# Kernel tuning notes

Measured on AMD Instinct MI355X. Metric: run time of the kernel, lower is better.

The kernel has to match this reference:

```python
import jax, jax.numpy as jnp
import numpy as np

D_IN, H, H1, H2 = 50, 64, 32, 1

def setup_inputs() -> dict:
    key = jax.random.key(0)
    ks = jax.random.split(key, 13)
    s = 1.0 / np.sqrt(H)
    u = lambda k, shp: jax.random.uniform(k, shp, jnp.float32, -s, s)
    x = jax.random.normal(ks[0], (512, 2048, D_IN), jnp.float32)
    return {
        "x": x,
        "W_ih0": u(ks[1], (H, D_IN)), "W_hh0": u(ks[2], (H, H)),
        "b_ih0": u(ks[3], (H,)),      "b_hh0": u(ks[4], (H,)),
        "W_ih1": u(ks[5], (H, H)),    "W_hh1": u(ks[6], (H, H)),
        "b_ih1": u(ks[7], (H,)),      "b_hh1": u(ks[8], (H,)),
        "W1": u(ks[9], (H1, H)),      "b1": u(ks[10], (H1,)),
        "W2": u(ks[11], (H2, H1)),    "b2": u(ks[12], (H2,)),
    }

def reference(x, W_ih0, W_hh0, b_ih0, b_hh0, W_ih1, W_hh1, b_ih1, b_hh1, W1, b1, W2, b2):
    B = x.shape[0]
    # Precompute input projections for layer 0 for all timesteps: [S, B, H]
    xt = jnp.swapaxes(x, 0, 1)  # [S, B, D_IN]
    x_proj0 = jnp.einsum('sbd,hd->sbh', xt, W_ih0) + b_ih0 + b_hh0

    h0 = jnp.zeros((B, H), x.dtype)

    def step(carry, xp):
        h1, h2 = carry
        h1 = jnp.tanh(xp + h1 @ W_hh0.T)
        h2 = jnp.tanh(h1 @ W_ih1.T + b_ih1 + h2 @ W_hh1.T + b_hh1)
        return (h1, h2), None

    (h1f, h2f), _ = jax.lax.scan(step, (h0, h0), x_proj0)
    hidden = jax.nn.relu(h2f @ W1.T + b1)
    return jax.nn.sigmoid(hidden @ W2.T + b2)
```

## Files before the change

kernel.cpp:

```cpp
#include <hip/hip_runtime.h>

#define S_LEN 2048
#define DIN   50
#define H     64

__device__ __forceinline__ float tanh_fast(float v) {
    float e = __builtin_amdgcn_exp2f(v * 2.885390082f);
    return 1.0f - 2.0f * __builtin_amdgcn_rcpf(e + 1.0f);
}

__device__ __forceinline__ float red4(float v) {
#if __has_builtin(__builtin_amdgcn_permlane16_swap) && __has_builtin(__builtin_amdgcn_permlane32_swap)
    typedef unsigned u2 __attribute__((ext_vector_type(2)));
    u2 r = __builtin_amdgcn_permlane16_swap(__float_as_uint(v), __float_as_uint(v), false, false);
    float s = __uint_as_float(r[0]) + __uint_as_float(r[1]);
    u2 q = __builtin_amdgcn_permlane32_swap(__float_as_uint(s), __float_as_uint(s), false, false);
    return __uint_as_float(q[0]) + __uint_as_float(q[1]);
#else
    v += __shfl_xor(v, 16, 64);
    v += __shfl_xor(v, 32, 64);
    return v;
#endif
}

__global__ __launch_bounds__(512)
__attribute__((amdgpu_waves_per_eu(4, 4)))
void rnn_fused(const float* __restrict__ x,
               const float* __restrict__ W_ih0, const float* __restrict__ W_hh0,
               const float* __restrict__ b_ih0, const float* __restrict__ b_hh0,
               const float* __restrict__ W_ih1, const float* __restrict__ W_hh1,
               const float* __restrict__ b_ih1, const float* __restrict__ b_hh1,
               const float* __restrict__ W1, const float* __restrict__ b1,
               const float* __restrict__ W2, const float* __restrict__ b2,
               float* __restrict__ out)
{
    const int b    = blockIdx.x;
    const int tid  = threadIdx.x;
    const int lane = tid & 63;
    const int w    = __builtin_amdgcn_readfirstlane(tid >> 6);
    const bool isA = (w < 4);
    const int wr   = isA ? w : w - 4;
    const int j    = lane & 15;
    const int kg   = lane >> 4;
    const int outj = 16 * wr + j;

    __shared__ __align__(16) float xs[2][4][16];
    __shared__ __align__(16) float h1s[2][H];
    __shared__ __align__(16) float h2s[2][H];

    float arrP[16], arrQ[16];
    if (isA) {
        #pragma unroll
        for (int i = 0; i < 16; ++i) {
            int c = 13 * kg + i;
            arrP[i] = (i < 13 && c < DIN) ? W_ih0[outj * DIN + c] : 0.0f;
            arrQ[i] = W_hh0[outj * H + 16 * kg + i];
        }
    } else {
        #pragma unroll
        for (int i = 0; i < 16; ++i) {
            arrP[i] = W_ih1[outj * H + 16 * kg + i];
            arrQ[i] = W_hh1[outj * H + 16 * kg + i];
        }
    }
    const float bias = isA ? (b_ih0[outj] + b_hh0[outj])
                           : (b_ih1[outj] + b_hh1[outj]);

    const float* __restrict__ xrow = x + (size_t)b * (size_t)(S_LEN * DIN);

    const int  scol = 13 * kg + j;
    const bool sval = (tid < 64) && (j < 13) && (scol < DIN);

    if (tid < 64) xs[0][kg][j] = sval ? xrow[scol] : 0.0f;
    float pfA = sval ? xrow[DIN + scol] : 0.0f;
    float pfB = sval ? xrow[2 * DIN + scol] : 0.0f;
    const float* xpf = xrow + 3 * DIN + scol;

    if (tid < 64) { h1s[1][lane] = 0.0f; h2s[1][lane] = 0.0f; }
    __syncthreads();

    auto iter = [&](int t, int cur, int prv) {
        if (isA) {
            if (t < S_LEN) {
                float s1[16], s2[16];
                #pragma unroll
                for (int q = 0; q < 4; ++q)
                    *(float4*)&s1[4 * q] = *(const float4*)&xs[cur][kg][4 * q];
                #pragma unroll
                for (int q = 0; q < 4; ++q)
                    *(float4*)&s2[4 * q] = *(const float4*)&h1s[prv][16 * kg + 4 * q];
                float a0 = 0, a1 = 0, a2 = 0, a3 = 0;
                #pragma unroll
                for (int q = 0; q < 4; ++q) {
                    a0 = fmaf(s1[4 * q + 0], arrP[4 * q + 0], a0);
                    a1 = fmaf(s1[4 * q + 1], arrP[4 * q + 1], a1);
                    a2 = fmaf(s1[4 * q + 2], arrP[4 * q + 2], a2);
                    a3 = fmaf(s1[4 * q + 3], arrP[4 * q + 3], a3);
                }
                #pragma unroll
                for (int q = 0; q < 4; ++q) {
                    a0 = fmaf(s2[4 * q + 0], arrQ[4 * q + 0], a0);
                    a1 = fmaf(s2[4 * q + 1], arrQ[4 * q + 1], a1);
                    a2 = fmaf(s2[4 * q + 2], arrQ[4 * q + 2], a2);
                    a3 = fmaf(s2[4 * q + 3], arrQ[4 * q + 3], a3);
                }
                float h1n = tanh_fast(red4((a0 + a1) + (a2 + a3)) + bias);
                if (kg == 0) h1s[cur][outj] = h1n;
                if (tid < 64) xs[prv][kg][j] = pfA;
                pfA = pfB;
                pfB = (sval && (t + 3) < S_LEN) ? *xpf : 0.0f;
                xpf += DIN;
            }
        } else {
            if (t >= 1) {
                float s1[16], s2[16];
                #pragma unroll
                for (int q = 0; q < 4; ++q)
                    *(float4*)&s1[4 * q] = *(const float4*)&h1s[prv][16 * kg + 4 * q];
                #pragma unroll
                for (int q = 0; q < 4; ++q)
                    *(float4*)&s2[4 * q] = *(const float4*)&h2s[cur][16 * kg + 4 * q];
                float c0 = 0, c1 = 0, c2 = 0, c3 = 0;
                #pragma unroll
                for (int q = 0; q < 4; ++q) {
                    c0 = fmaf(s1[4 * q + 0], arrP[4 * q + 0], c0);
                    c1 = fmaf(s1[4 * q + 1], arrP[4 * q + 1], c1);
                    c2 = fmaf(s1[4 * q + 2], arrP[4 * q + 2], c2);
                    c3 = fmaf(s1[4 * q + 3], arrP[4 * q + 3], c3);
                }
                #pragma unroll
                for (int q = 0; q < 4; ++q) {
                    c0 = fmaf(s2[4 * q + 0], arrQ[4 * q + 0], c0);
                    c1 = fmaf(s2[4 * q + 1], arrQ[4 * q + 1], c1);
                    c2 = fmaf(s2[4 * q + 2], arrQ[4 * q + 2], c2);
                    c3 = fmaf(s2[4 * q + 3], arrQ[4 * q + 3], c3);
                }
                float h2n = tanh_fast(red4((c0 + c1) + (c2 + c3)) + bias);
                if (kg == 0) h2s[prv][outj] = h2n;
            }
        }
    };

    for (int t = 0; t < S_LEN; t += 2) {
        iter(t, 0, 1);
        __syncthreads();
        iter(t + 1, 1, 0);
        __syncthreads();
    }
    iter(S_LEN, 0, 1);
    __syncthreads();

    if (tid < 64) {
        float hv = 0.0f;
        if (lane < 32) {
            float acc = b1[lane];
            #pragma unroll
            for (int k = 0; k < H; ++k)
                acc = fmaf(h2s[1][k], W1[lane * H + k], acc);
            hv = fmaxf(acc, 0.0f) * W2[lane];
        }
        #pragma unroll
        for (int off = 32; off; off >>= 1)
            hv += __shfl_xor(hv, off, 64);
        if (lane == 0)
            out[b] = 1.0f / (1.0f + __expf(-(hv + b2[0])));
    }
}

extern "C" void kernel_launch(void* const* d_in, const int* in_sizes, int n_in,
                              void* d_out, int out_size, void* d_ws, size_t ws_size,
                              hipStream_t stream) {
    const float* x     = (const float*)d_in[0];
    const float* W_ih0 = (const float*)d_in[1];
    const float* W_hh0 = (const float*)d_in[2];
    const float* b_ih0 = (const float*)d_in[3];
    const float* b_hh0 = (const float*)d_in[4];
    const float* W_ih1 = (const float*)d_in[5];
    const float* W_hh1 = (const float*)d_in[6];
    const float* b_ih1 = (const float*)d_in[7];
    const float* b_hh1 = (const float*)d_in[8];
    const float* W1    = (const float*)d_in[9];
    const float* b1    = (const float*)d_in[10];
    const float* W2    = (const float*)d_in[11];
    const float* b2    = (const float*)d_in[12];
    float* out = (float*)d_out;

    rnn_fused<<<dim3(512), dim3(512), 0, stream>>>(
        x, W_ih0, W_hh0, b_ih0, b_hh0,
        W_ih1, W_hh1, b_ih1, b_hh1,
        W1, b1, W2, b2, out);
}
```

Before: 1.087 ms.

## Rewrite RNN recurrence as single-wave bf16 MFMA kernel batching 16 sequences

Replaces the 512-thread-per-sequence FP32 dot-product kernel with a one-wavefront block that handles 16 batch rows and runs both RNN layers through bf16 16x16x32 MFMA instructions. Weights are held as bf16 register fragments, and hidden states go through a small LDS transpose each step to re-form A fragments. The next x projection is computed one step ahead and inputs are prefetched from global memory. This removes block-wide barriers and cuts the grid from 512 to 32 blocks. The cost is bf16 rounding of weights and hidden states across 2048 steps, plus very low parallelism (32 waves) on a large GPU.

Measured after the change: 1.900 ms. 74.8% more time.

```diff
diff --git a/kernel.cpp b/kernel.cpp
--- a/kernel.cpp
+++ b/kernel.cpp
@@ -3,6 +3,33 @@
 #define S_LEN 2048
 #define DIN   50
 #define H     64
+#define ROWS  16
+#define XSTR  (S_LEN * DIN)
+
+typedef short bf16x8 __attribute__((ext_vector_type(8)));
+typedef float f32x4  __attribute__((ext_vector_type(4)));
+
+union U8 { bf16x8 v; unsigned u[4]; };
+
+__device__ __forceinline__ unsigned cvt2bf(float lo, float hi) {
+    unsigned r;
+    asm("v_cvt_pk_bf16_f32 %0, %1, %2" : "=v"(r) : "v"(lo), "v"(hi));
+    return r;
+}
+
+__device__ __forceinline__ bf16x8 pack8v(float4 a, float4 b) {
+    U8 u;
+    u.u[0] = cvt2bf(a.x, a.y); u.u[1] = cvt2bf(a.z, a.w);
+    u.u[2] = cvt2bf(b.x, b.y); u.u[3] = cvt2bf(b.z, b.w);
+    return u.v;
+}
+
+__device__ __forceinline__ bf16x8 pack8a(const float f[8]) {
+    U8 u;
+    u.u[0] = cvt2bf(f[0], f[1]); u.u[1] = cvt2bf(f[2], f[3]);
+    u.u[2] = cvt2bf(f[4], f[5]); u.u[3] = cvt2bf(f[6], f[7]);
+    return u.v;
+}
 
 __device__ __forceinline__ float tanh_fast(float v) {
     float e = __builtin_amdgcn_exp2f(v * 2.885390082f);
@@ -23,147 +50,204 @@
 #endif
 }
 
-__global__ __launch_bounds__(512)
-__attribute__((amdgpu_waves_per_eu(4, 4)))
-void rnn_fused(const float* __restrict__ x,
-               const float* __restrict__ W_ih0, const float* __restrict__ W_hh0,
-               const float* __restrict__ b_ih0, const float* __restrict__ b_hh0,
-               const float* __restrict__ W_ih1, const float* __restrict__ W_hh1,
-               const float* __restrict__ b_ih1, const float* __restrict__ b_hh1,
-               const float* __restrict__ W1, const float* __restrict__ b1,
-               const float* __restrict__ W2, const float* __restrict__ b2,
-               float* __restrict__ out)
+__device__ __forceinline__ bf16x8 load_bfrag(const float* __restrict__ W, int ld, int kmax,
+                                             int n, int ks) {
+    float f[8];
+    #pragma unroll
+    for (int j = 0; j < 8; ++j)
+        f[j] = (ks + j < kmax) ? W[n * ld + ks + j] : 0.0f;
+    return pack8a(f);
+}
+
+#define MFMA(a, b, c) __builtin_amdgcn_mfma_f32_16x16x32_bf16(a, b, c, 0, 0, 0)
+
+__global__ __launch_bounds__(64)
+__attribute__((amdgpu_waves_per_eu(1, 1)))
+void rnn_mfma(const float* __restrict__ x,
+              const float* __restrict__ W_ih0, const float* __restrict__ W_hh0,
+              const float* __restrict__ b_ih0, const float* __restrict__ b_hh0,
+              const float* __restrict__ W_ih1, const float* __restrict__ W_hh1,
+              const float* __restrict__ b_ih1, const float* __restrict__ b_hh1,
+              const float* __restrict__ W1, const float* __restrict__ b1,
+              const float* __restrict__ W2, const float* __restrict__ b2,
+              float* __restrict__ out)
 {
-    const int b    = blockIdx.x;
-    const int tid  = threadIdx.x;
-    const int lane = tid & 63;
-    const int w    = __builtin_amdgcn_readfirstlane(tid >> 6);
-    const bool isA = (w < 4);
-    const int wr   = isA ? w : w - 4;
-    const int j    = lane & 15;
-    const int kg   = lane >> 4;
-    const int outj = 16 * wr + j;
-
-    __shared__ __align__(16) float xs[2][4][16];
-    __shared__ __align__(16) float h1s[2][H];
-    __shared__ __align__(16) float h2s[2][H];
-
-    float arrP[16], arrQ[16];
-    if (isA) {
-        #pragma unroll
-        for (int i = 0; i < 16; ++i) {
-            int c = 13 * kg + i;
-            arrP[i] = (i < 13 && c < DIN) ? W_ih0[outj * DIN + c] : 0.0f;
-            arrQ[i] = W_hh0[outj * H + 16 * kg + i];
-        }
-    } else {
-        #pragma unroll
-        for (int i = 0; i < 16; ++i) {
-            arrP[i] = W_ih1[outj * H + 16 * kg + i];
-            arrQ[i] = W_hh1[outj * H + 16 * kg + i];
-        }
-    }
-    const float bias = isA ? (b_ih0[outj] + b_hh0[outj])
-                           : (b_ih1[outj] + b_hh1[outj]);
-
-    const float* __restrict__ xrow = x + (size_t)b * (size_t)(S_LEN * DIN);
-
-    const int  scol = 13 * kg + j;
-    const bool sval = (tid < 64) && (j < 13) && (scol < DIN);
-
-    if (tid < 64) xs[0][kg][j] = sval ? xrow[scol] : 0.0f;
-    float pfA = sval ? xrow[DIN + scol] : 0.0f;
-    float pfB = sval ? xrow[2 * DIN + scol] : 0.0f;
-    const float* xpf = xrow + 3 * DIN + scol;
-
-    if (tid < 64) { h1s[1][lane] = 0.0f; h2s[1][lane] = 0.0f; }
-    __syncthreads();
-
-    auto iter = [&](int t, int cur, int prv) {
-        if (isA) {
-            if (t < S_LEN) {
-                float s1[16], s2[16];
-                #pragma unroll
-                for (int q = 0; q < 4; ++q)
-                    *(float4*)&s1[4 * q] = *(const float4*)&xs[cur][kg][4 * q];
-                #pragma unroll
-                for (int q = 0; q < 4; ++q)
-                    *(float4*)&s2[4 * q] = *(const float4*)&h1s[prv][16 * kg + 4 * q];
-                float a0 = 0, a1 = 0, a2 = 0, a3 = 0;
-                #pragma unroll
-                for (int q = 0; q < 4; ++q) {
-                    a0 = fmaf(s1[4 * q + 0], arrP[4 * q + 0], a0);
-                    a1 = fmaf(s1[4 * q + 1], arrP[4 * q + 1], a1);
-                    a2 = fmaf(s1[4 * q + 2], arrP[4 * q + 2], a2);
-                    a3 = fmaf(s1[4 * q + 3], arrP[4 * q + 3], a3);
-                }
-                #pragma unroll
-                for (int q = 0; q < 4; ++q) {
-                    a0 = fmaf(s2[4 * q + 0], arrQ[4 * q + 0], a0);
-                    a1 = fmaf(s2[4 * q + 1], arrQ[4 * q + 1], a1);
-                    a2 = fmaf(s2[4 * q + 2], arrQ[4 * q + 2], a2);
-                    a3 = fmaf(s2[4 * q + 3], arrQ[4 * q + 3], a3);
-                }
-                float h1n = tanh_fast(red4((a0 + a1) + (a2 + a3)) + bias);
-                if (kg == 0) h1s[cur][outj] = h1n;
-                if (tid < 64) xs[prv][kg][j] = pfA;
-                pfA = pfB;
-                pfB = (sval && (t + 3) < S_LEN) ? *xpf : 0.0f;
-                xpf += DIN;
-            }
-        } else {
-            if (t >= 1) {
-                float s1[16], s2[16];
-                #pragma unroll
-                for (int q = 0; q < 4; ++q)
-                    *(float4*)&s1[4 * q] = *(const float4*)&h1s[prv][16 * kg + 4 * q];
-                #pragma unroll
-                for (int q = 0; q < 4; ++q)
-                    *(float4*)&s2[4 * q] = *(const float4*)&h2s[cur][16 * kg + 4 * q];
-                float c0 = 0, c1 = 0, c2 = 0, c3 = 0;
-                #pragma unroll
-                for (int q = 0; q < 4; ++q) {
-                    c0 = fmaf(s1[4 * q + 0], arrP[4 * q + 0], c0);
-                    c1 = fmaf(s1[4 * q + 1], arrP[4 * q + 1], c1);
-                    c2 = fmaf(s1[4 * q + 2], arrP[4 * q + 2], c2);
-                    c3 = fmaf(s1[4 * q + 3], arrP[4 * q + 3], c3);
-                }
-                #pragma unroll
-                for (int q = 0; q < 4; ++q) {
-                    c0 = fmaf(s2[4 * q + 0], arrQ[4 * q + 0], c0);
-                    c1 = fmaf(s2[4 * q + 1], arrQ[4 * q + 1], c1);
-                    c2 = fmaf(s2[4 * q + 2], arrQ[4 * q + 2], c2);
-                    c3 = fmaf(s2[4 * q + 3], arrQ[4 * q + 3], c3);
-                }
-                float h2n = tanh_fast(red4((c0 + c1) + (c2 + c3)) + bias);
-                if (kg == 0) h2s[prv][outj] = h2n;
-            }
-        }
-    };
-
-    for (int t = 0; t < S_LEN; t += 2) {
-        iter(t, 0, 1);
-        __syncthreads();
-        iter(t + 1, 1, 0);
-        __syncthreads();
-    }
-    iter(S_LEN, 0, 1);
-    __syncthreads();
-
-    if (tid < 64) {
-        float hv = 0.0f;
-        if (lane < 32) {
-            float acc = b1[lane];
-            #pragma unroll
-            for (int k = 0; k < H; ++k)
-                acc = fmaf(h2s[1][k], W1[lane * H + k], acc);
-            hv = fmaxf(acc, 0.0f) * W2[lane];
-        }
-        #pragma unroll
-        for (int off = 32; off; off >>= 1)
-            hv += __shfl_xor(hv, off, 64);
-        if (lane == 0)
-            out[b] = 1.0f / (1.0f + __expf(-(hv + b2[0])));
+    const int blk  = blockIdx.x;
+    const int lane = threadIdx.x & 63;
+    const int li   = lane & 15;
+    const int lg   = lane >> 4;
+
+    __shared__ __align__(16) float hb1[ROWS][68];
+    __shared__ __align__(16) float hb2[ROWS][68];
+
+    bf16x8 whh0B[4][2], wih1B[4][2], whh1B[4][2], wih0B[4][2];
+    f32x4  b0c[4], b1c[4];
+    #pragma unroll
+    for (int nt = 0; nt < 4; ++nt) {
+        const int n = 16 * nt + li;
+        #pragma unroll
+        for (int kf = 0; kf < 2; ++kf) {
+            const int ks = 32 * kf + lg * 8;
+            whh0B[nt][kf] = load_bfrag(W_hh0, H,   H,   n, ks);
+            wih1B[nt][kf] = load_bfrag(W_ih1, H,   H,   n, ks);
+            whh1B[nt][kf] = load_bfrag(W_hh1, H,   H,   n, ks);
+            wih0B[nt][kf] = load_bfrag(W_ih0, DIN, DIN, n, ks);
+        }
+        const float v0 = b_ih0[n] + b_hh0[n];
+        const float v1 = b_ih1[n] + b_hh1[n];
+        b0c[nt] = f32x4{v0, v0, v0, v0};
+        b1c[nt] = f32x4{v1, v1, v1, v1};
+    }
+
+    const float* __restrict__ xbase = x + (size_t)(ROWS * blk + li) * XSTR + lg * 8;
+
+    float xr0[8], xr1[8];
+    bf16x8 xfragA[2];
+    bf16x8 h1frag[2] = {bf16x8{0,0,0,0,0,0,0,0}, bf16x8{0,0,0,0,0,0,0,0}};
+    bf16x8 h2frag[2] = {bf16x8{0,0,0,0,0,0,0,0}, bf16x8{0,0,0,0,0,0,0,0}};
+    f32x4  xpacc[4];
+
+    {
+        float f0[8], f1[8];
+        #pragma unroll
+        for (int m = 0; m < 4; ++m) {
+            float2 a = *(const float2*)(xbase + 2 * m);
+            f0[2*m] = a.x; f0[2*m+1] = a.y;
+            float2 b = *(const float2*)(xbase + 32 + 2 * m);
+            f1[2*m] = b.x; f1[2*m+1] = b.y;
+        }
+        bf16x8 x0f0 = pack8a(f0), x0f1 = pack8a(f1);
+        #pragma unroll
+        for (int nt = 0; nt < 4; ++nt) {
+            xpacc[nt] = MFMA(x0f0, wih0B[nt][0], b0c[nt]);
+            xpacc[nt] = MFMA(x0f1, wih0B[nt][1], xpacc[nt]);
+        }
+        #pragma unroll
+        for (int m = 0; m < 4; ++m) {
+            float2 a = *(const float2*)(xbase + 50 + 2 * m);
+            f0[2*m] = a.x; f0[2*m+1] = a.y;
+            float2 b = *(const float2*)(xbase + 50 + 32 + 2 * m);
+            f1[2*m] = b.x; f1[2*m+1] = b.y;
+        }
+        xfragA[0] = pack8a(f0); xfragA[1] = pack8a(f1);
+        #pragma unroll
+        for (int m = 0; m < 4; ++m) {
+            float2 a = *(const float2*)(xbase + 100 + 2 * m);
+            xr0[2*m] = a.x; xr0[2*m+1] = a.y;
+            float2 b = *(const float2*)(xbase + 100 + 32 + 2 * m);
+            xr1[2*m] = b.x; xr1[2*m+1] = b.y;
+        }
+    }
+
+    float xn0[8], xn1[8];
+    #pragma unroll
+    for (int j = 0; j < 8; ++j) { xn0[j] = 0.0f; xn1[j] = 0.0f; }
+
+    #pragma unroll 2
+    for (int t = 0; t < S_LEN; ++t) {
+        f32x4 acc2[4];
+        #pragma unroll
+        for (int nt = 0; nt < 4; ++nt) {
+            acc2[nt] = MFMA(h2frag[0], whh1B[nt][0], b1c[nt]);
+            acc2[nt] = MFMA(h2frag[1], whh1B[nt][1], acc2[nt]);
+        }
+        f32x4 acc1[4];
+        #pragma unroll
+        for (int nt = 0; nt < 4; ++nt) {
+            acc1[nt] = MFMA(h1frag[0], whh0B[nt][0], xpacc[nt]);
+            acc1[nt] = MFMA(h1frag[1], whh0B[nt][1], acc1[nt]);
+        }
+        #pragma unroll
+        for (int nt = 0; nt < 4; ++nt) {
+            xpacc[nt] = MFMA(xfragA[0], wih0B[nt][0], b0c[nt]);
+            xpacc[nt] = MFMA(xfragA[1], wih0B[nt][1], xpacc[nt]);
+        }
+        const int t3 = t + 3;
+        if (t3 <= S_LEN - 2) {
+            const float* p = xbase + t3 * DIN;
+            #pragma unroll
+            for (int m = 0; m < 4; ++m) {
+                float2 a = *(const float2*)(p + 2 * m);
+                xn0[2*m] = a.x; xn0[2*m+1] = a.y;
+                float2 b = *(const float2*)(p + 32 + 2 * m);
+                xn1[2*m] = b.x; xn1[2*m+1] = b.y;
+            }
+        } else if (t3 == S_LEN - 1) {
+            const float* p = xbase + t3 * DIN;
+            #pragma unroll
+            for (int m = 0; m < 4; ++m) {
+                float2 a = *(const float2*)(p + 2 * m);
+                xn0[2*m] = a.x; xn0[2*m+1] = a.y;
+            }
+            #pragma unroll
+            for (int j = 0; j < 8; ++j) {
+                const int k = 32 + lg * 8 + j;
+                xn1[j] = (k < DIN) ? p[32 + j] : 0.0f;
+            }
+        }
+        #pragma unroll
+        for (int nt = 0; nt < 4; ++nt)
+            #pragma unroll
+            for (int i = 0; i < 4; ++i)
+                hb1[lg * 4 + i][16 * nt + li] = tanh_fast(acc1[nt][i]);
+        {
+            float4 a0 = *(const float4*)&hb1[li][lg * 8];
+            float4 a1 = *(const float4*)&hb1[li][lg * 8 + 4];
+            float4 c0 = *(const float4*)&hb1[li][32 + lg * 8];
+            float4 c1 = *(const float4*)&hb1[li][32 + lg * 8 + 4];
+            h1frag[0] = pack8v(a0, a1);
+            h1frag[1] = pack8v(c0, c1);
+        }
+        #pragma unroll
+        for (int nt = 0; nt < 4; ++nt) {
+            acc2[nt] = MFMA(h1frag[0], wih1B[nt][0], acc2[nt]);
+            acc2[nt] = MFMA(h1frag[1], wih1B[nt][1], acc2[nt]);
+        }
+        #pragma unroll
+        for (int nt = 0; nt < 4; ++nt)
+            #pragma unroll
+            for (int i = 0; i < 4; ++i)
+                hb2[lg * 4 + i][16 * nt + li] = tanh_fast(acc2[nt][i]);
+        {
+            float4 a0 = *(const float4*)&hb2[li][lg * 8];
+            float4 a1 = *(const float4*)&hb2[li][lg * 8 + 4];
+            float4 c0 = *(const float4*)&hb2[li][32 + lg * 8];
+            float4 c1 = *(const float4*)&hb2[li][32 + lg * 8 + 4];
+            h2frag[0] = pack8v(a0, a1);
+            h2frag[1] = pack8v(c0, c1);
+        }
+        {
+            float q0[8], q1[8];
+            #pragma unroll
+            for (int j = 0; j < 8; ++j) { q0[j] = xr0[j]; q1[j] = xr1[j]; }
+            xfragA[0] = pack8a(q0);
+            xfragA[1] = pack8a(q1);
+            #pragma unroll
+            for (int j = 0; j < 8; ++j) { xr0[j] = xn0[j]; xr1[j] = xn1[j]; }
+        }
+    }
+
+    {
+        const int r = li, qg = lg;
+        float part = 0.0f;
+        #pragma unroll
+        for (int jj = 0; jj < 8; ++jj) {
+            const int q = 8 * qg + jj;
+            float a = b1[q];
+            const float4* w4 = (const float4*)(W1 + q * H);
+            #pragma unroll
+            for (int kq = 0; kq < 16; ++kq) {
+                float4 wv = w4[kq];
+                a = fmaf(hb2[r][4*kq+0], wv.x, a);
+                a = fmaf(hb2[r][4*kq+1], wv.y, a);
+                a = fmaf(hb2[r][4*kq+2], wv.z, a);
+                a = fmaf(hb2[r][4*kq+3], wv.w, a);
+            }
+            part = fmaf(fmaxf(a, 0.0f), W2[q], part);
+        }
+        float tot = red4(part);
+        if (lane < ROWS)
+            out[ROWS * blk + lane] = 1.0f / (1.0f + __expf(-(tot + b2[0])));
     }
 }
 
@@ -185,7 +269,7 @@
     const float* b2    = (const float*)d_in[12];
     float* out = (float*)d_out;
 
-    rnn_fused<<<dim3(512), dim3(512), 0, stream>>>(
+    rnn_mfma<<<dim3(512 / ROWS), dim3(64), 0, stream>>>(
         x, W_ih0, W_hh0, b_ih0, b_hh0,
         W_ih1, W_hh1, b_ih1, b_hh1,
         W1, b1, W2, b2, out);
```
